# Optimization experiments

Hardware: AMD Instinct MI355X
Metric: run time of the kernel (lower is better)

The kernel has to match this reference:

```python
import jax, jax.numpy as jnp
import numpy as np

S, B, D, H = 2048, 2, 1024, 16
DK = D // H


def setup_inputs() -> dict:
    key = jax.random.key(0)
    k1, k2, k3 = jax.random.split(key, 3)
    x = jax.random.normal(k1, (S, B, D), dtype=jnp.float32)
    # xavier-uniform-like scale for weights
    w_qkv = jax.random.normal(k2, (3 * D, D), dtype=jnp.float32) * (1.0 / np.sqrt(D))
    w_out = jax.random.normal(k3, (D, D), dtype=jnp.float32) * (1.0 / np.sqrt(D))
    b_out = jnp.zeros((D,), dtype=jnp.float32)
    return {"x": x, "w_qkv": w_qkv, "w_out": w_out, "b_out": b_out}


def reference(x, w_qkv, w_out, b_out):
    seq_len, batch, d_model = x.shape
    n_heads = H
    d_k = d_model // n_heads
    # qkv projection: [S,B,3D]
    qkv = jnp.einsum('sbd,ed->sbe', x, w_qkv)
    qkv = qkv.reshape(seq_len, batch, 3, n_heads, d_k)
    qkv = jnp.transpose(qkv, (2, 1, 3, 0, 4))  # [3,B,H,S,dk]
    q, k, v = qkv[0], qkv[1], qkv[2]
    scores = jnp.einsum('bhqd,bhkd->bhqk', q, k) / jnp.sqrt(jnp.asarray(d_k, x.dtype))
    causal = jnp.triu(jnp.ones((seq_len, seq_len), dtype=bool), k=1)
    scores = jnp.where(causal[None, None], jnp.asarray(-jnp.inf, scores.dtype), scores)
    weights = jax.nn.softmax(scores, axis=-1)
    out = jnp.einsum('bhqk,bhkd->bhqd', weights, v)  # [B,H,S,dk]
    out = jnp.transpose(out, (2, 0, 1, 3)).reshape(seq_len, batch, d_model)
    return jnp.einsum('sbd,ed->sbe', out, w_out) + b_out
```

## Files before the change

### kernel.cpp

```cpp
#include <hip/hip_runtime.h>
#include <cstdint>

typedef _Float16 f16;
typedef _Float16 f16x4 __attribute__((ext_vector_type(4)));
typedef _Float16 f16x8 __attribute__((ext_vector_type(8)));
typedef float f32x4 __attribute__((ext_vector_type(4)));

#define MFMA16(a, b, c) __builtin_amdgcn_mfma_f32_16x16x32_f16(a, b, c, 0, 0, 0)
#define QSCALE 0.1803368801111243f

__device__ __forceinline__ void gload_lds16(const void* g, void* l) {
    __builtin_amdgcn_global_load_lds((__attribute__((address_space(1))) void*)(g),
                                     (__attribute__((address_space(3))) void*)(l),
                                     16, 0, 0);
}


__global__ void cast_all(const float* __restrict__ x, const float* __restrict__ wqv,
                         const float* __restrict__ wo, f16* __restrict__ out) {
    int i = blockIdx.x * blockDim.x + threadIdx.x;
    const float* src; int li;
    if (i < 1048576)      { src = x;   li = i; }
    else if (i < 1835008) { src = wqv; li = i - 1048576; }
    else                  { src = wo;  li = i - 1835008; }
    float4 v = reinterpret_cast<const float4*>(src)[li];
    f16x4 o = {(f16)v.x, (f16)v.y, (f16)v.z, (f16)v.w};
    reinterpret_cast<f16x4*>(out)[i] = o;
}

__global__ __launch_bounds__(256) void gemm_qkv(
    const f16* __restrict__ A, const f16* __restrict__ B,
    f16* __restrict__ outq, f16* __restrict__ outk, f16* __restrict__ outvt)
{
    __shared__ f16 SM[128 * 64 * 2];
    f16* As = SM;
    f16* Bs = SM + 8192;
    const int tid = threadIdx.x;
    const int lane = tid & 63;
    const int wave = tid >> 6;
    const int wm = wave >> 1, wn = wave & 1;
    const int bm = blockIdx.y * 128, bn = blockIdx.x * 128;
    const int sr = tid >> 3;
    const int scu = (tid & 7) ^ (sr & 7);
    const int fr = lane & 15, fq = lane >> 4;
    const int u0 = (fq ^ (fr & 7)) * 8;
    const int u1 = ((4 + fq) ^ (fr & 7)) * 8;

    f32x4 acc[4][4] = {};

    for (int k0 = 0; k0 < 1024; k0 += 64) {
        __syncthreads();
#pragma unroll
        for (int is = 0; is < 4; ++is) {
            gload_lds16(&A[(bm + sr + is * 32) * 1024 + k0 + scu * 8], &As[is * 2048 + tid * 8]);
            gload_lds16(&B[(bn + sr + is * 32) * 1024 + k0 + scu * 8], &Bs[is * 2048 + tid * 8]);
        }
        __syncthreads();
        f16x8 af0[4], af1[4], bf0[4], bf1[4];
#pragma unroll
        for (int mt = 0; mt < 4; ++mt) {
            int r = wm * 64 + mt * 16 + fr;
            af0[mt] = *(const f16x8*)&As[r * 64 + u0];
            af1[mt] = *(const f16x8*)&As[r * 64 + u1];
        }
#pragma unroll
        for (int nt = 0; nt < 4; ++nt) {
            int r = wn * 64 + nt * 16 + fr;
            bf0[nt] = *(const f16x8*)&Bs[r * 64 + u0];
            bf1[nt] = *(const f16x8*)&Bs[r * 64 + u1];
        }
#pragma unroll
        for (int mt = 0; mt < 4; ++mt)
#pragma unroll
            for (int nt = 0; nt < 4; ++nt) {
                acc[mt][nt] = MFMA16(af0[mt], bf0[nt], acc[mt][nt]);
                acc[mt][nt] = MFMA16(af1[mt], bf1[nt], acc[mt][nt]);
            }
    }

    const int x = blockIdx.x;
    if (x < 16) {
        f16* base = (x < 8) ? outq : outk;
        const float scale = (x < 8) ? QSCALE : 1.0f;
        const int coloff = (x < 8) ? bn : (bn - 1024);
#pragma unroll
        for (int mt = 0; mt < 4; ++mt)
#pragma unroll
            for (int nt = 0; nt < 4; ++nt)
#pragma unroll
                for (int i = 0; i < 4; ++i) {
                    int row = bm + wm * 64 + mt * 16 + fq * 4 + i;
                    int col = coloff + wn * 64 + nt * 16 + fr;
                    int s = row >> 1, b = row & 1;
                    int h = col >> 6, dk = col & 63;
                    base[((b * 16 + h) * 2048 + s) * 64 + dk] = (f16)(acc[mt][nt][i] * scale);
                }
    } else {
        const int xb = x - 16;
        const int s0 = bm >> 1;
        f16* Ts = SM;
#pragma unroll
        for (int p = 0; p < 2; ++p) {
            __syncthreads();
            if (wn == p) {
#pragma unroll
                for (int mt = 0; mt < 4; ++mt)
#pragma unroll
                    for (int nt = 0; nt < 4; ++nt)
#pragma unroll
                        for (int i = 0; i < 4; ++i) {
                            int row = wm * 64 + mt * 16 + fq * 4 + i;
                            int cl = nt * 16 + fr;
                            Ts[(cl * 2 + (row & 1)) * 76 + (row >> 1)] = (f16)acc[mt][nt][i];
                        }
            }
            __syncthreads();
            const int h = xb * 2 + p;
            const int sj = tid & 7;
#pragma unroll
            for (int it = 0; it < 4; ++it) {
                int idx = (tid >> 3) + it * 32;
                int bsel = idx & 1, dk = idx >> 1;
                f16x8 v = *(const f16x8*)&Ts[(dk * 2 + bsel) * 76 + sj * 8];
                *(f16x8*)&outvt[((bsel * 16 + h) * 64 + dk) * 2048 + s0 + sj * 8] = v;
            }
        }
    }
}

__global__ __launch_bounds__(256) void attn_kernel(
    const f16* __restrict__ qg, const f16* __restrict__ kg,
    const f16* __restrict__ vtg, f16* __restrict__ attn)
{
    __shared__ f16 Ks[2][64 * 64];
    __shared__ f16 Vs[2][64 * 64];
    __shared__ f16 plds[4][16 * 72];
    const int tid = threadIdx.x;
    const int lane = tid & 63;
    const int wave = tid >> 6;
    const int qpair = blockIdx.x;
    const int bh = blockIdx.y;
    const int b = bh >> 4, h = bh & 15;
    const int fr = lane & 15, fq = lane >> 4;

    const int bqA = qpair * 64;
    const int bqB = (31 - qpair) * 64;
    const int nA = qpair + 1;
    const int nB = 32 - qpair;
    const int qrowA = bqA + wave * 16;
    const int qrowB = bqB + wave * 16;

    const f16* Q  = qg  + bh * 2048 * 64;
    const f16* K  = kg  + bh * 2048 * 64;
    const f16* VT = vtg + bh * 64 * 2048;
    f16* P = plds[wave];

    const int sr = tid >> 3;
    const int scu = (tid & 7) ^ (sr & 7);

    f16x8 aqA0 = *(const f16x8*)&Q[(qrowA + fr) * 64 + fq * 8];
    f16x8 aqA1 = *(const f16x8*)&Q[(qrowA + fr) * 64 + 32 + fq * 8];
    f16x8 aqB0 = *(const f16x8*)&Q[(qrowB + fr) * 64 + fq * 8];
    f16x8 aqB1 = *(const f16x8*)&Q[(qrowB + fr) * 64 + 32 + fq * 8];

    f32x4 oA[4] = {}, oB[4] = {};
    float lA[4] = {}, lB[4] = {};

    auto stage = [&](int kc, int buf) {
        const int kb = kc * 64;
        gload_lds16(&K[(kb + sr) * 64 + scu * 8],         &Ks[buf][tid * 8]);
        gload_lds16(&K[(kb + sr + 32) * 64 + scu * 8],    &Ks[buf][2048 + tid * 8]);
        gload_lds16(&VT[sr * 2048 + kb + scu * 8],        &Vs[buf][tid * 8]);
        gload_lds16(&VT[(sr + 32) * 2048 + kb + scu * 8], &Vs[buf][2048 + tid * 8]);
    };

    auto compute = [&](const f16x8& aq0, const f16x8& aq1, int qrow0, int kb,
                       const f16* Ksb, const f16* Vsb, f32x4* oacc, float* li, bool domask) {
        f32x4 sc[4] = {};
#pragma unroll
        for (int ct = 0; ct < 4; ++ct) {
            int r = ct * 16 + fr;
            f16x8 b0 = *(const f16x8*)&Ksb[r * 64 + ((fq ^ (r & 7)) * 8)];
            f16x8 b1 = *(const f16x8*)&Ksb[r * 64 + (((4 + fq) ^ (r & 7)) * 8)];
            sc[ct] = MFMA16(aq0, b0, sc[ct]);
            sc[ct] = MFMA16(aq1, b1, sc[ct]);
        }
        if (domask) {
#pragma unroll
            for (int ct = 0; ct < 4; ++ct) {
                int kcol = kb + ct * 16 + fr;
#pragma unroll
                for (int i = 0; i < 4; ++i)
                    if (kcol > qrow0 + fq * 4 + i) sc[ct][i] = -1e30f;
            }
        }
#pragma unroll
        for (int i = 0; i < 4; ++i) {
            float p0 = __builtin_amdgcn_exp2f(sc[0][i]);
            float p1 = __builtin_amdgcn_exp2f(sc[1][i]);
            float p2 = __builtin_amdgcn_exp2f(sc[2][i]);
            float p3 = __builtin_amdgcn_exp2f(sc[3][i]);
            li[i] += (p0 + p1) + (p2 + p3);
            P[(fq * 4 + i) * 72 + fr]      = (f16)p0;
            P[(fq * 4 + i) * 72 + 16 + fr] = (f16)p1;
            P[(fq * 4 + i) * 72 + 32 + fr] = (f16)p2;
            P[(fq * 4 + i) * 72 + 48 + fr] = (f16)p3;
        }
        f16x8 ap0 = *(const f16x8*)&P[fr * 72 + fq * 8];
        f16x8 ap1 = *(const f16x8*)&P[fr * 72 + 32 + fq * 8];
#pragma unroll
        for (int nt = 0; nt < 4; ++nt) {
            int dk = nt * 16 + fr;
            f16x8 bv0 = *(const f16x8*)&Vsb[dk * 64 + ((fq ^ (dk & 7)) * 8)];
            f16x8 bv1 = *(const f16x8*)&Vsb[dk * 64 + (((4 + fq) ^ (dk & 7)) * 8)];
            oacc[nt] = MFMA16(ap0, bv0, oacc[nt]);
            oacc[nt] = MFMA16(ap1, bv1, oacc[nt]);
        }
    };

    stage(0, 0);
    for (int kc = 0; kc < nB; ++kc) {
        const int kb = kc * 64;
        const int cur = kc & 1;
        __syncthreads();
        if (kc + 1 < nB) stage(kc + 1, cur ^ 1);
        compute(aqB0, aqB1, qrowB, kb, Ks[cur], Vs[cur], oB, lB, kb + 63 > qrowB);
        if (kc < nA)
            compute(aqA0, aqA1, qrowA, kb, Ks[cur], Vs[cur], oA, lA, kb + 63 > qrowA);
    }

#pragma unroll
    for (int i = 0; i < 4; ++i) {
        float rs = lA[i];
        rs += __shfl_xor(rs, 1);
        rs += __shfl_xor(rs, 2);
        rs += __shfl_xor(rs, 4);
        rs += __shfl_xor(rs, 8);
        float inv = __builtin_amdgcn_rcpf(rs);
        int srow = qrowA + fq * 4 + i;
#pragma unroll
        for (int nt = 0; nt < 4; ++nt)
            attn[(srow * 2 + b) * 1024 + h * 64 + nt * 16 + fr] = (f16)(oA[nt][i] * inv);
    }
#pragma unroll
    for (int i = 0; i < 4; ++i) {
        float rs = lB[i];
        rs += __shfl_xor(rs, 1);
        rs += __shfl_xor(rs, 2);
        rs += __shfl_xor(rs, 4);
        rs += __shfl_xor(rs, 8);
        float inv = __builtin_amdgcn_rcpf(rs);
        int srow = qrowB + fq * 4 + i;
#pragma unroll
        for (int nt = 0; nt < 4; ++nt)
            attn[(srow * 2 + b) * 1024 + h * 64 + nt * 16 + fr] = (f16)(oB[nt][i] * inv);
    }
}

__global__ __launch_bounds__(256) void gemm_out(
    const f16* __restrict__ A, const f16* __restrict__ B,
    const float* __restrict__ bias, float* __restrict__ out)
{
    __shared__ f16 As[128 * 64];
    __shared__ f16 Bs[64 * 64];
    const int tid = threadIdx.x;
    const int lane = tid & 63;
    const int wave = tid >> 6;
    const int wm = wave >> 1, wn = wave & 1;
    const int bm = blockIdx.y * 128, bn = blockIdx.x * 64;
    const int sr = tid >> 3;
    const int scu = (tid & 7) ^ (sr & 7);
    const int fr = lane & 15, fq = lane >> 4;
    const int u0 = (fq ^ (fr & 7)) * 8;
    const int u1 = ((4 + fq) ^ (fr & 7)) * 8;

    f32x4 acc[4][2] = {};

    for (int k0 = 0; k0 < 1024; k0 += 64) {
        __syncthreads();
#pragma unroll
        for (int is = 0; is < 4; ++is)
            gload_lds16(&A[(bm + sr + is * 32) * 1024 + k0 + scu * 8], &As[is * 2048 + tid * 8]);
#pragma unroll
        for (int is = 0; is < 2; ++is)
            gload_lds16(&B[(bn + sr + is * 32) * 1024 + k0 + scu * 8], &Bs[is * 2048 + tid * 8]);
        __syncthreads();
        f16x8 af0[4], af1[4], bf0[2], bf1[2];
#pragma unroll
        for (int mt = 0; mt < 4; ++mt) {
            int r = wm * 64 + mt * 16 + fr;
            af0[mt] = *(const f16x8*)&As[r * 64 + u0];
            af1[mt] = *(const f16x8*)&As[r * 64 + u1];
        }
#pragma unroll
        for (int nt = 0; nt < 2; ++nt) {
            int r = wn * 32 + nt * 16 + fr;
            bf0[nt] = *(const f16x8*)&Bs[r * 64 + u0];
            bf1[nt] = *(const f16x8*)&Bs[r * 64 + u1];
        }
#pragma unroll
        for (int mt = 0; mt < 4; ++mt)
#pragma unroll
            for (int nt = 0; nt < 2; ++nt) {
                acc[mt][nt] = MFMA16(af0[mt], bf0[nt], acc[mt][nt]);
                acc[mt][nt] = MFMA16(af1[mt], bf1[nt], acc[mt][nt]);
            }
    }

#pragma unroll
    for (int mt = 0; mt < 4; ++mt)
#pragma unroll
        for (int nt = 0; nt < 2; ++nt)
#pragma unroll
            for (int i = 0; i < 4; ++i) {
                int row = bm + wm * 64 + mt * 16 + fq * 4 + i;
                int col = bn + wn * 32 + nt * 16 + fr;
                out[row * 1024 + col] = acc[mt][nt][i] + bias[col];
            }
}

extern "C" void kernel_launch(void* const* d_in, const int* in_sizes, int n_in,
                              void* d_out, int out_size, void* d_ws, size_t ws_size,
                              hipStream_t stream)
{
    const float* x     = (const float*)d_in[0];
    const float* w_qkv = (const float*)d_in[1];
    const float* w_out = (const float*)d_in[2];
    const float* b_out = (const float*)d_in[3];
    float* out = (float*)d_out;

    char* ws = (char*)d_ws;
    f16* xh  = (f16*)(ws);
    f16* wqh = (f16*)(ws + 8388608);
    f16* woh = (f16*)(ws + 14680064);
    f16* qh  = (f16*)(ws + 16777216);
    f16* kh  = (f16*)(ws + 25165824);
    f16* vt  = (f16*)(ws + 33554432);
    f16* ah  = (f16*)(ws + 41943040);

    cast_all<<<8192, 256, 0, stream>>>(x, w_qkv, w_out, xh);
    gemm_qkv<<<dim3(24, 32), 256, 0, stream>>>(xh, wqh, qh, kh, vt);
    attn_kernel<<<dim3(16, 32), 256, 0, stream>>>(qh, kh, vt, ah);
    gemm_out<<<dim3(16, 32), 256, 0, stream>>>(ah, woh, b_out, out);
}
```

Baseline: 187.5 us.

## Split attention query tiles across 8 waves instead of serial pair per wave

The attention block now launches 512 threads, with waves 0-3 handling the late query tile (B) and waves 4-7 the early tile (A), instead of each of 4 waves computing both tiles one after the other. Each thread stages half as many K/V chunks into LDS, and the per-wave P buffer grows to 8 slots. This aims to raise parallelism and latency hiding per CU and to cut per-thread register pressure. The cost is load imbalance: the A waves go idle at the barriers once their short key range is done, and fewer blocks may fit on each CU.

```diff
diff --git a/kernel.cpp b/kernel.cpp
--- a/kernel.cpp
+++ b/kernel.cpp
@@ -128,13 +128,13 @@
     }
 }
 
-__global__ __launch_bounds__(256) void attn_kernel(
+__global__ __launch_bounds__(512) void attn_kernel(
     const f16* __restrict__ qg, const f16* __restrict__ kg,
     const f16* __restrict__ vtg, f16* __restrict__ attn)
 {
     __shared__ f16 Ks[2][64 * 64];
     __shared__ f16 Vs[2][64 * 64];
-    __shared__ f16 plds[4][16 * 72];
+    __shared__ f16 plds[8][16 * 72];
     const int tid = threadIdx.x;
     const int lane = tid & 63;
     const int wave = tid >> 6;
@@ -143,12 +143,11 @@
     const int b = bh >> 4, h = bh & 15;
     const int fr = lane & 15, fq = lane >> 4;
 
-    const int bqA = qpair * 64;
-    const int bqB = (31 - qpair) * 64;
-    const int nA = qpair + 1;
+    const bool isB = wave < 4;
+    const int w4 = wave & 3;
+    const int qrow = (isB ? (31 - qpair) : qpair) * 64 + w4 * 16;
     const int nB = 32 - qpair;
-    const int qrowA = bqA + wave * 16;
-    const int qrowB = bqB + wave * 16;
+    const int nK = isB ? nB : (qpair + 1);
 
     const f16* Q  = qg  + bh * 2048 * 64;
     const f16* K  = kg  + bh * 2048 * 64;
@@ -158,24 +157,19 @@
     const int sr = tid >> 3;
     const int scu = (tid & 7) ^ (sr & 7);
 
-    f16x8 aqA0 = *(const f16x8*)&Q[(qrowA + fr) * 64 + fq * 8];
-    f16x8 aqA1 = *(const f16x8*)&Q[(qrowA + fr) * 64 + 32 + fq * 8];
-    f16x8 aqB0 = *(const f16x8*)&Q[(qrowB + fr) * 64 + fq * 8];
-    f16x8 aqB1 = *(const f16x8*)&Q[(qrowB + fr) * 64 + 32 + fq * 8];
-
-    f32x4 oA[4] = {}, oB[4] = {};
-    float lA[4] = {}, lB[4] = {};
+    f16x8 aq0 = *(const f16x8*)&Q[(qrow + fr) * 64 + fq * 8];
+    f16x8 aq1 = *(const f16x8*)&Q[(qrow + fr) * 64 + 32 + fq * 8];
+
+    f32x4 o[4] = {};
+    float l[4] = {};
 
     auto stage = [&](int kc, int buf) {
         const int kb = kc * 64;
-        gload_lds16(&K[(kb + sr) * 64 + scu * 8],         &Ks[buf][tid * 8]);
-        gload_lds16(&K[(kb + sr + 32) * 64 + scu * 8],    &Ks[buf][2048 + tid * 8]);
-        gload_lds16(&VT[sr * 2048 + kb + scu * 8],        &Vs[buf][tid * 8]);
-        gload_lds16(&VT[(sr + 32) * 2048 + kb + scu * 8], &Vs[buf][2048 + tid * 8]);
+        gload_lds16(&K[(kb + sr) * 64 + scu * 8], &Ks[buf][tid * 8]);
+        gload_lds16(&VT[sr * 2048 + kb + scu * 8], &Vs[buf][tid * 8]);
     };
 
-    auto compute = [&](const f16x8& aq0, const f16x8& aq1, int qrow0, int kb,
-                       const f16* Ksb, const f16* Vsb, f32x4* oacc, float* li, bool domask) {
+    auto compute = [&](int kb, const f16* Ksb, const f16* Vsb, bool domask) {
         f32x4 sc[4] = {};
 #pragma unroll
         for (int ct = 0; ct < 4; ++ct) {
@@ -191,7 +185,7 @@
                 int kcol = kb + ct * 16 + fr;
 #pragma unroll
                 for (int i = 0; i < 4; ++i)
-                    if (kcol > qrow0 + fq * 4 + i) sc[ct][i] = -1e30f;
+                    if (kcol > qrow + fq * 4 + i) sc[ct][i] = -1e30f;
             }
         }
 #pragma unroll
@@ -200,7 +194,7 @@
             float p1 = __builtin_amdgcn_exp2f(sc[1][i]);
             float p2 = __builtin_amdgcn_exp2f(sc[2][i]);
             float p3 = __builtin_amdgcn_exp2f(sc[3][i]);
-            li[i] += (p0 + p1) + (p2 + p3);
+            l[i] += (p0 + p1) + (p2 + p3);
             P[(fq * 4 + i) * 72 + fr]      = (f16)p0;
             P[(fq * 4 + i) * 72 + 16 + fr] = (f16)p1;
             P[(fq * 4 + i) * 72 + 32 + fr] = (f16)p2;
@@ -213,8 +207,8 @@
             int dk = nt * 16 + fr;
             f16x8 bv0 = *(const f16x8*)&Vsb[dk * 64 + ((fq ^ (dk & 7)) * 8)];
             f16x8 bv1 = *(const f16x8*)&Vsb[dk * 64 + (((4 + fq) ^ (dk & 7)) * 8)];
-            oacc[nt] = MFMA16(ap0, bv0, oacc[nt]);
-            oacc[nt] = MFMA16(ap1, bv1, oacc[nt]);
+            o[nt] = MFMA16(ap0, bv0, o[nt]);
+            o[nt] = MFMA16(ap1, bv1, o[nt]);
         }
     };
 
@@ -224,36 +218,21 @@
         const int cur = kc & 1;
         __syncthreads();
         if (kc + 1 < nB) stage(kc + 1, cur ^ 1);
-        compute(aqB0, aqB1, qrowB, kb, Ks[cur], Vs[cur], oB, lB, kb + 63 > qrowB);
-        if (kc < nA)
-            compute(aqA0, aqA1, qrowA, kb, Ks[cur], Vs[cur], oA, lA, kb + 63 > qrowA);
+        if (kc < nK) compute(kb, Ks[cur], Vs[cur], kb + 63 > qrow);
     }
 
 #pragma unroll
     for (int i = 0; i < 4; ++i) {
-        float rs = lA[i];
+        float rs = l[i];
         rs += __shfl_xor(rs, 1);
         rs += __shfl_xor(rs, 2);
         rs += __shfl_xor(rs, 4);
         rs += __shfl_xor(rs, 8);
         float inv = __builtin_amdgcn_rcpf(rs);
-        int srow = qrowA + fq * 4 + i;
+        int srow = qrow + fq * 4 + i;
 #pragma unroll
         for (int nt = 0; nt < 4; ++nt)
-            attn[(srow * 2 + b) * 1024 + h * 64 + nt * 16 + fr] = (f16)(oA[nt][i] * inv);
-    }
-#pragma unroll
-    for (int i = 0; i < 4; ++i) {
-        float rs = lB[i];
-        rs += __shfl_xor(rs, 1);
-        rs += __shfl_xor(rs, 2);
-        rs += __shfl_xor(rs, 4);
-        rs += __shfl_xor(rs, 8);
-        float inv = __builtin_amdgcn_rcpf(rs);
-        int srow = qrowB + fq * 4 + i;
-#pragma unroll
-        for (int nt = 0; nt < 4; ++nt)
-            attn[(srow * 2 + b) * 1024 + h * 64 + nt * 16 + fr] = (f16)(oB[nt][i] * inv);
+            attn[(srow * 2 + b) * 1024 + h * 64 + nt * 16 + fr] = (f16)(o[nt][i] * inv);
     }
 }
 
@@ -340,6 +319,6 @@
 
     cast_all<<<8192, 256, 0, stream>>>(x, w_qkv, w_out, xh);
     gemm_qkv<<<dim3(24, 32), 256, 0, stream>>>(xh, wqh, qh, kh, vt);
-    attn_kernel<<<dim3(16, 32), 256, 0, stream>>>(qh, kh, vt, ah);
+    attn_kernel<<<dim3(16, 32), 512, 0, stream>>>(qh, kh, vt, ah);
     gemm_out<<<dim3(16, 32), 256, 0, stream>>>(ah, woh, b_out, out);
 }
```

Measured after the change: 178.7 us. -4.7%, faster.
